# Performance work log

Measured on AMD Instinct MI355X. Metric: run time of the kernel, lower is better.

Reference implementation:

```python
import jax, jax.numpy as jnp
import numpy as np

D_MODEL = 2048
N_HEADS = 16
D_KEY = D_MODEL // N_HEADS
ALIBI_SLOPE = 8.0
KEY_SCALE = D_KEY ** -0.5
B, S = 2, 2048


def setup_inputs() -> dict:
    key = jax.random.key(0)
    ks = jax.random.split(key, 12)
    sd = D_MODEL ** -0.5
    return {
        "states": jax.random.normal(ks[0], (B, S, D_MODEL), jnp.float32),
        "bias_mask": jax.random.normal(ks[1], (B, S, S), jnp.float32),
        # weights stored [in, out] (torch Linear applies x @ W.T + b)
        "wq": jax.random.normal(ks[2], (D_MODEL, D_MODEL), jnp.float32) * sd,
        "bq": jnp.zeros((D_MODEL,), jnp.float32),
        "wk": jax.random.normal(ks[3], (D_MODEL, D_MODEL), jnp.float32) * sd,
        "bk": jnp.zeros((D_MODEL,), jnp.float32),
        "wv": jax.random.normal(ks[4], (D_MODEL, D_MODEL), jnp.float32) * sd,
        "bv": jnp.zeros((D_MODEL,), jnp.float32),
        "wg": jax.random.normal(ks[5], (D_MODEL, N_HEADS), jnp.float32) * sd,
        "bg": jnp.zeros((N_HEADS,), jnp.float32),
        "wo": jax.random.normal(ks[6], (D_MODEL, D_MODEL), jnp.float32) * sd,
        "bo": jnp.zeros((D_MODEL,), jnp.float32),
    }


def reference(states, bias_mask, wq, bq, wk, bk, wv, bv, wg, bg, wo, bo):
    # head_scale = exp2(-(h+1)*alibi_slope/n_heads), non-trainable buffer
    head_scale = jnp.exp2(-(jnp.arange(N_HEADS, dtype=jnp.float32) + 1.0)
                          * ALIBI_SLOPE / N_HEADS)
    # [B, H, Q, K] bias with per-head ALiBi scaling
    bias = bias_mask[:, None, :, :] * head_scale[None, :, None, None]

    def heads(x, w, b):  # [B,S,D] -> [B,H,S,Dk]
        y = x @ w + b
        return y.reshape(x.shape[0], x.shape[1], N_HEADS, D_KEY).transpose(0, 2, 1, 3)

    q = heads(states, wq, bq)
    k = heads(states, wk, bk)
    v = heads(states, wv, bv)

    scores = jnp.einsum('bhqd,bhkd->bhqk', q, k) * KEY_SCALE + bias
    probs = jax.nn.softmax(scores, axis=-1)
    o = jnp.einsum('bhqk,bhkd->bqhd', probs, v)  # [B,S,H,Dk]

    g = jax.nn.sigmoid(states @ wg + bg)  # [B,S,H] head gate
    o = o * g[..., None]

    return o.reshape(o.shape[0], o.shape[1], D_MODEL) @ wo + bo
```

## Files before the change

### kernel.cpp

```cpp
#include <hip/hip_runtime.h>
#include <hip/hip_bf16.h>

#define SEQ 2048
#define DM 2048
#define NH 16
#define DK 128
#define LOG2E 1.4426950408889634f
#define QK_SCALE 0.08838834764831845f

typedef __attribute__((ext_vector_type(8))) short short8;
typedef __attribute__((ext_vector_type(4))) float f32x4;
typedef __attribute__((ext_vector_type(4))) unsigned short us4;

__device__ __forceinline__ unsigned short f2b(float f) {
  union { float f; unsigned u; } v; v.f = f;
  unsigned r = v.u + 0x7fffu + ((v.u >> 16) & 1u);
  return (unsigned short)(r >> 16);
}
__device__ __forceinline__ float b2f(unsigned short v) {
  union { unsigned u; float f; } x; x.u = ((unsigned)v) << 16; return x.f;
}

__device__ __forceinline__ void gl_lds16(const void* g, void* l) {
  __builtin_amdgcn_global_load_lds((const __attribute__((address_space(1))) void*)g,
                                   (__attribute__((address_space(3))) void*)l, 16, 0, 0);
}

#define SBAR()   __builtin_amdgcn_s_barrier()
#define SCHED0() __builtin_amdgcn_sched_barrier(0)
#define LGKM0()  asm volatile("s_waitcnt lgkmcnt(0)" ::: "memory")

__global__ __launch_bounds__(256) void cast_bf16_kernel(const float* __restrict__ in,
                                                        unsigned short* __restrict__ out) {
  int i = blockIdx.x * 256 + threadIdx.x;
  const float4* p = (const float4*)in;
  float4 a = p[2*i], b = p[2*i+1];
  us4 r0, r1;
  r0[0]=f2b(a.x); r0[1]=f2b(a.y); r0[2]=f2b(a.z); r0[3]=f2b(a.w);
  r1[0]=f2b(b.x); r1[1]=f2b(b.y); r1[2]=f2b(b.z); r1[3]=f2b(b.w);
  us4* o = (us4*)out;
  o[2*i] = r0; o[2*i+1] = r1;
}

__global__ __launch_bounds__(256) void transpose_cast4_kernel(const float* __restrict__ w0,
                                                              const float* __restrict__ w1,
                                                              const float* __restrict__ w2,
                                                              const float* __restrict__ w3,
                                                              unsigned short* __restrict__ dst) {
  const float* w = (blockIdx.z == 0) ? w0 : (blockIdx.z == 1) ? w1 : (blockIdx.z == 2) ? w2 : w3;
  unsigned short* wt = dst + (size_t)blockIdx.z * DM * DM;
  __shared__ float t[64][65];
  int c0 = blockIdx.x * 64, r0 = blockIdx.y * 64;
  int tid = threadIdx.x;
  int rr = tid >> 4;
  int c4 = (tid & 15) * 4;
#pragma unroll
  for (int p = 0; p < 4; ++p) {
    int r = p*16 + rr;
    float4 v = *(const float4*)&w[(size_t)(r0 + r)*DM + c0 + c4];
    t[r][c4] = v.x; t[r][c4+1] = v.y; t[r][c4+2] = v.z; t[r][c4+3] = v.w;
  }
  __syncthreads();
#pragma unroll
  for (int p = 0; p < 4; ++p) {
    int c = p*16 + rr;
    us4 v;
    v[0] = f2b(t[c4+0][c]); v[1] = f2b(t[c4+1][c]);
    v[2] = f2b(t[c4+2][c]); v[3] = f2b(t[c4+3][c]);
    *(us4*)&wt[(size_t)(c0 + c)*DM + r0 + c4] = v;
  }
}

__global__ __launch_bounds__(256) void transpose_wg_kernel(const float* __restrict__ wg,
                                                           unsigned short* __restrict__ wgT) {
  int idx = blockIdx.x * 256 + threadIdx.x;
  int c = idx & 15;
  int r0 = (idx >> 4) * 4;
#pragma unroll
  for (int r = 0; r < 4; ++r)
    wgT[(size_t)c*DM + r0 + r] = f2b(wg[(size_t)(r0 + r)*NH + c]);
}

__device__ __forceinline__ void gemm256_core(const unsigned short* __restrict__ A,
                                             const unsigned short* __restrict__ Bt,
                                             int m0, int n0, f32x4 (&acc)[8][4]) {
  __shared__ __align__(16) unsigned short Ab[2][2][8192];
  __shared__ __align__(16) unsigned short Bb[2][2][8192];
  const int TK = DM / 64;

  int tid = threadIdx.x, wid = tid >> 6, lane = tid & 63;
  int lo = lane & 15, hi = lane >> 4;
  int wm = wid >> 2, wn = wid & 3;
  int w2 = wid * 2;

  int srow8 = lane >> 3;
  int skb = (((lane & 7) ^ srow8) << 4);
  const char* Ag = (const char*)A;
  const char* Bg = (const char*)Bt;

#define STG_A(S,CUR) do {                                                          \
    const char* g = Ag + (size_t)(S)*128 + skb;                                    \
    char* l = (char*)&Ab[CUR][0][0] + w2*1024;                                     \
    gl_lds16(g + (size_t)(m0 + w2*8 + srow8)*4096,           l);                   \
    gl_lds16(g + (size_t)(m0 + w2*8 + 8 + srow8)*4096,       l + 1024);            \
    gl_lds16(g + (size_t)(m0 + 128 + w2*8 + srow8)*4096,     l + 16384);           \
    gl_lds16(g + (size_t)(m0 + 128 + w2*8 + 8 + srow8)*4096, l + 16384 + 1024);    \
  } while(0)
#define STG_B(S,CUR) do {                                                          \
    const char* g = Bg + (size_t)(S)*128 + skb;                                    \
    char* l = (char*)&Bb[CUR][0][0] + w2*1024;                                     \
    gl_lds16(g + (size_t)(n0 + w2*8 + srow8)*4096,           l);                   \
    gl_lds16(g + (size_t)(n0 + w2*8 + 8 + srow8)*4096,       l + 1024);            \
    gl_lds16(g + (size_t)(n0 + 128 + w2*8 + srow8)*4096,     l + 16384);           \
    gl_lds16(g + (size_t)(n0 + 128 + w2*8 + 8 + srow8)*4096, l + 16384 + 1024);    \
  } while(0)

#pragma unroll
  for (int i = 0; i < 8; ++i)
#pragma unroll
    for (int j = 0; j < 4; ++j) acc[i][j] = (f32x4){0.f,0.f,0.f,0.f};

  STG_B(0,0); STG_A(0,0); STG_B(1,1); STG_A(1,1);
  asm volatile("s_waitcnt vmcnt(8)" ::: "memory");
  SBAR();

  int msk = (lo & 7) << 4;
  int k0 = (hi*16) ^ msk;
  int k1 = (64 + hi*16) ^ msk;
  int brow = (wn & 1) * 64;

  short8 a[4][2], bA[2][2], bB[2][2];

#define MF16(MH,NH,BF)                                                              \
  __builtin_amdgcn_s_setprio(1);                                                    \
  _Pragma("unroll") for (int mm = 0; mm < 4; ++mm)                                  \
  _Pragma("unroll") for (int nn = 0; nn < 2; ++nn) {                                \
    acc[(MH)*4+mm][(NH)*2+nn] = __builtin_amdgcn_mfma_f32_16x16x32_bf16(            \
        a[mm][0], BF[nn][0], acc[(MH)*4+mm][(NH)*2+nn], 0, 0, 0);                   \
    acc[(MH)*4+mm][(NH)*2+nn] = __builtin_amdgcn_mfma_f32_16x16x32_bf16(            \
        a[mm][1], BF[nn][1], acc[(MH)*4+mm][(NH)*2+nn], 0, 0, 0);                   \
  }                                                                                 \
  __builtin_amdgcn_s_setprio(0);

  for (int s = 0; s < TK; ++s) {
    int cur = s & 1;
    const char* Ac = (const char*)&Ab[cur][wm][0];
    const char* Bc = (const char*)&Bb[cur][wn >> 1][0];
    bool pre = (s + 2) < TK;

#pragma unroll
    for (int mm = 0; mm < 4; ++mm) {
      a[mm][0] = *(const short8*)(Ac + (mm*16 + lo)*128 + k0);
      a[mm][1] = *(const short8*)(Ac + (mm*16 + lo)*128 + k1);
    }
#pragma unroll
    for (int nn = 0; nn < 2; ++nn) {
      bA[nn][0] = *(const short8*)(Bc + (brow + nn*16 + lo)*128 + k0);
      bA[nn][1] = *(const short8*)(Bc + (brow + nn*16 + lo)*128 + k1);
    }
    SBAR(); LGKM0(); SCHED0();
    MF16(0, 0, bA);
    SBAR();

#pragma unroll
    for (int nn = 0; nn < 2; ++nn) {
      bB[nn][0] = *(const short8*)(Bc + (brow + (2+nn)*16 + lo)*128 + k0);
      bB[nn][1] = *(const short8*)(Bc + (brow + (2+nn)*16 + lo)*128 + k1);
    }
    SBAR(); LGKM0(); SCHED0();
    MF16(0, 1, bB);
    SBAR();

#pragma unroll
    for (int mm = 0; mm < 4; ++mm) {
      a[mm][0] = *(const short8*)(Ac + ((64 + mm*16 + lo)*128) + k0);
      a[mm][1] = *(const short8*)(Ac + ((64 + mm*16 + lo)*128) + k1);
    }
    if (pre) STG_B(s + 2, cur);
    SBAR(); LGKM0(); SCHED0();
    MF16(1, 0, bA);
    SBAR();

    if (pre) {
      STG_A(s + 2, cur);
      asm volatile("s_waitcnt vmcnt(8)" ::: "memory");
    } else if (s == TK - 2) {
      asm volatile("s_waitcnt vmcnt(0)" ::: "memory");
    }
    SBAR();
    MF16(1, 1, bB);
    SBAR();
  }
#undef STG_A
#undef STG_B
#undef MF16
}

__global__ __launch_bounds__(512, 2) void gemm256_qkv_kernel(const unsigned short* __restrict__ A,
                                                             const unsigned short* __restrict__ Bt,
                                                             const float* __restrict__ bq,
                                                             const float* __restrict__ bk,
                                                             const float* __restrict__ bv,
                                                             unsigned short* __restrict__ QB,
                                                             unsigned short* __restrict__ KB,
                                                             unsigned short* __restrict__ VTB) {
  f32x4 acc[8][4];
  int bid = blockIdx.x;
  int orig = (bid & 7) * 48 + (bid >> 3);
  int n0 = (orig % 24) * 256, m0 = (orig / 24) * 256;
  gemm256_core(A, Bt, m0, n0, acc);

  int tid = threadIdx.x, wid = tid >> 6, lane = tid & 63;
  int lo = lane & 15, hi = lane >> 4;
  int wm = wid >> 2, wn = wid & 3;
  int sect = n0 >> 11;

  if (sect == 2) {
#pragma unroll
    for (int mi = 0; mi < 8; ++mi) {
      int m = m0 + wm*128 + mi*16 + 4*hi;
      int b = m >> 11, srow = m & 2047;
#pragma unroll
      for (int nf = 0; nf < 4; ++nf) {
        int n = n0 + wn*64 + nf*16 + lo;
        int nl = n & 2047, h = nl >> 7, d = nl & 127;
        float bvv = bv[nl];
        us4 pk;
#pragma unroll
        for (int r = 0; r < 4; ++r) pk[r] = f2b(acc[mi][nf][r] + bvv);
        *(us4*)&VTB[(((size_t)(b*NH + h))*DK + d)*SEQ + srow] = pk;
      }
    }
  } else {
    unsigned short* out = sect ? KB : QB;
    const float* bp = sect ? bk : bq;
    const float qs = sect ? 1.f : QK_SCALE * LOG2E;
#pragma unroll
    for (int mi = 0; mi < 8; ++mi) {
#pragma unroll
      for (int nf = 0; nf < 4; ++nf) {
        int n = n0 + wn*64 + nf*16 + lo;
        int nl = n & 2047, h = nl >> 7, d = nl & 127;
        float bvv = bp[nl];
#pragma unroll
        for (int r = 0; r < 4; ++r) {
          int m = m0 + wm*128 + mi*16 + 4*hi + r;
          int b = m >> 11, srow = m & 2047;
          out[(((size_t)(b*NH + h))*SEQ + srow)*DK + d] = f2b((acc[mi][nf][r] + bvv) * qs);
        }
      }
    }
  }
}

__global__ __launch_bounds__(512, 2) void gemm256_ao_kernel(const unsigned short* __restrict__ A,
                                                            const unsigned short* __restrict__ Bt,
                                                            const float* __restrict__ bias,
                                                            float* __restrict__ out) {
  f32x4 acc[8][4];
  int bid = blockIdx.x;
  int orig = (bid & 7) * 16 + (bid >> 3);
  int n0 = (orig & 7) * 256, m0 = (orig >> 3) * 256;
  gemm256_core(A, Bt, m0, n0, acc);

  int tid = threadIdx.x, wid = tid >> 6, lane = tid & 63;
  int lo = lane & 15, hi = lane >> 4;
  int wm = wid >> 2, wn = wid & 3;
#pragma unroll
  for (int mi = 0; mi < 8; ++mi) {
#pragma unroll
    for (int nf = 0; nf < 4; ++nf) {
      int n = n0 + wn*64 + nf*16 + lo;
      float bvv = bias[n];
#pragma unroll
      for (int r = 0; r < 4; ++r) {
        int m = m0 + wm*128 + mi*16 + 4*hi + r;
        out[(size_t)m*DM + n] = acc[mi][nf][r] + bvv;
      }
    }
  }
}

__global__ __launch_bounds__(256) void gate_mfma_kernel(const unsigned short* __restrict__ XB,
                                                        const unsigned short* __restrict__ wgT,
                                                        const float* __restrict__ bg,
                                                        float* __restrict__ G) {
  int tid = threadIdx.x, wid = tid >> 6, lane = tid & 63;
  int lo = lane & 15, hi = lane >> 4;
  int m0 = blockIdx.x * 64 + wid * 16;

  f32x4 acc = {0.f, 0.f, 0.f, 0.f};
  const unsigned short* xrow = XB + (size_t)(m0 + lo) * DM + hi * 8;
  const unsigned short* grow = wgT + (size_t)lo * DM + hi * 8;
#pragma unroll 4
  for (int kt = 0; kt < DM; kt += 32) {
    short8 a = *(const short8*)(xrow + kt);
    short8 b = *(const short8*)(grow + kt);
    acc = __builtin_amdgcn_mfma_f32_16x16x32_bf16(a, b, acc, 0, 0, 0);
  }
  float bgv = bg[lo];
#pragma unroll
  for (int r = 0; r < 4; ++r) {
    float x = acc[r] + bgv;
    G[(size_t)(m0 + 4*hi + r) * NH + lo] = 1.f / (1.f + __builtin_amdgcn_exp2f(-x * LOG2E));
  }
}

__global__ __attribute__((amdgpu_flat_work_group_size(512,512)))
__attribute__((amdgpu_waves_per_eu(2,4)))
void attn_kernel(const unsigned short* __restrict__ Q,
                 const unsigned short* __restrict__ Kb,
                 const unsigned short* __restrict__ VT,
                 const unsigned short* __restrict__ biasb,
                 const float* __restrict__ G,
                 unsigned short* __restrict__ OG) {
  __shared__ __align__(16) unsigned short kbuf[2][64*128];
  __shared__ __align__(16) unsigned short vbuf[2][128*64];
  __shared__ __align__(16) unsigned short pbuf[8*16*64];

  int bid = blockIdx.x;
  int h  = bid & 15;
  int b  = (bid >> 4) & 1;
  int qt = bid >> 5;
  int bh = b*NH + h;

  int tid = threadIdx.x, wid = tid >> 6, lane = tid & 63;
  int lo = lane & 15, hi = lane >> 4;
  int qw0 = qt*128 + wid*16;

  float hs2 = __builtin_amdgcn_exp2f(-(float)(h+1) * 0.5f) * LOG2E;

  short8 qf[4];
#pragma unroll
  for (int ks = 0; ks < 4; ++ks)
    qf[ks] = *(const short8*)&Q[((size_t)bh*SEQ + qw0 + lo)*DK + ks*32 + hi*8];

  f32x4 zero4 = {0.f,0.f,0.f,0.f};
  f32x4 acco[8];
#pragma unroll
  for (int f = 0; f < 8; ++f) acco[f] = zero4;
  float lrun[4];
#pragma unroll
  for (int r = 0; r < 4; ++r) lrun[r] = 0.f;

  const char* kbase = (const char*)Kb + ((size_t)bh*SEQ)*DK*2;
  const char* vbase = (const char*)VT + ((size_t)bh*DK)*SEQ*2;
  const unsigned short* bb = biasb + ((size_t)b*SEQ + qw0 + 4*hi)*SEQ + lo;
  char* pb = (char*)pbuf + wid*2048;

  int s16 = lane >> 4, srow8 = lane >> 3;
  int kof = (lane & 15) * 16, vof = (lane & 7) * 16;
  int w2 = wid * 2;

#define STAGE_KV(KT, BUF) do {                                                        \
    _Pragma("unroll")                                                                 \
    for (int c = 0; c < 2; ++c) {                                                     \
      int krc = (w2 + c)*4 + s16;                                                     \
      gl_lds16(kbase + (size_t)((KT) + krc)*256 + (kof ^ ((krc & 7) << 4)),           \
               (char*)kbuf[BUF] + (w2 + c)*1024);                                     \
      int vrc = (w2 + c)*8 + srow8;                                                   \
      gl_lds16(vbase + (size_t)vrc*4096 + (size_t)(KT)*2 + (vof ^ (srow8 << 4)),      \
               (char*)vbuf[BUF] + (w2 + c)*1024);                                     \
    }                                                                                 \
  } while(0)

  unsigned short br[4][4];
#pragma unroll
  for (int r = 0; r < 4; ++r)
#pragma unroll
    for (int nf = 0; nf < 4; ++nf)
      br[r][nf] = bb[(size_t)r*SEQ + nf*16];
  STAGE_KV(0, 0);
  STAGE_KV(64, 1);
  asm volatile("s_waitcnt vmcnt(4)" ::: "memory");
  SBAR();

  const int NT = SEQ / 64;
  int cur = 0;
  for (int t = 0; t < NT; ++t) {
    f32x4 sf[4];
    __builtin_amdgcn_s_setprio(1);
#pragma unroll
    for (int nf = 0; nf < 4; ++nf) {
      f32x4 a = zero4;
#pragma unroll
      for (int ks = 0; ks < 4; ++ks) {
        int krw = nf*16 + lo;
        int cb = (ks*32 + hi*8)*2;
        short8 kf = *(const short8*)((const char*)kbuf[cur] + krw*256 + (cb ^ ((krw & 7) << 4)));
        a = __builtin_amdgcn_mfma_f32_16x16x32_bf16(qf[ks], kf, a, 0, 0, 0);
      }
      sf[nf] = a;
    }
    __builtin_amdgcn_s_setprio(0);

#pragma unroll
    for (int r = 0; r < 4; ++r) {
      int prow = 4*hi + r;
#pragma unroll
      for (int nf = 0; nf < 4; ++nf) {
        float s = fmaf(b2f(br[r][nf]), hs2, sf[nf][r]);
        float p = __builtin_amdgcn_exp2f(s);
        lrun[r] += p;
        *(unsigned short*)(pb + prow*128 + ((((nf*16 + lo)*2)) ^ ((prow & 7) << 4))) = f2b(p);
      }
    }

    short8 pf[2];
#pragma unroll
    for (int ks = 0; ks < 2; ++ks)
      pf[ks] = *(const short8*)(pb + lo*128 + ((ks*64 + hi*16) ^ ((lo & 7) << 4)));
    __builtin_amdgcn_s_setprio(1);
#pragma unroll
    for (int f = 0; f < 8; ++f) {
#pragma unroll
      for (int ks = 0; ks < 2; ++ks) {
        int vrw = f*16 + lo;
        int cb = (ks*32 + hi*8)*2;
        short8 vf = *(const short8*)((const char*)vbuf[cur] + vrw*128 + (cb ^ ((vrw & 7) << 4)));
        acco[f] = __builtin_amdgcn_mfma_f32_16x16x32_bf16(pf[ks], vf, acco[f], 0, 0, 0);
      }
    }
    __builtin_amdgcn_s_setprio(0);

    LGKM0(); SBAR();

    bool more1 = (t + 1) < NT;
    bool more2 = (t + 2) < NT;
    if (more1) {
      int ktn = (t + 1) * 64;
#pragma unroll
      for (int r = 0; r < 4; ++r)
#pragma unroll
        for (int nf = 0; nf < 4; ++nf)
          br[r][nf] = bb[(size_t)r*SEQ + ktn + nf*16];
    }
    if (more2) {
      STAGE_KV((t + 2) * 64, cur);
      asm volatile("s_waitcnt vmcnt(20)" ::: "memory");
    } else if (more1) {
      asm volatile("s_waitcnt vmcnt(16)" ::: "memory");
    }
    SBAR();
    cur ^= 1;
  }
#undef STAGE_KV

#pragma unroll
  for (int r = 0; r < 4; ++r) {
    float l = lrun[r];
    l += __shfl_xor(l, 1); l += __shfl_xor(l, 2);
    l += __shfl_xor(l, 4); l += __shfl_xor(l, 8);
    lrun[r] = l;
  }

#pragma unroll
  for (int r = 0; r < 4; ++r) {
    int qrow = qw0 + 4*hi + r;
    float inv = 1.f / lrun[r];
    float g = G[((size_t)(b*SEQ + qrow))*NH + h];
    float sgl = inv * g;
#pragma unroll
    for (int f = 0; f < 8; ++f)
      OG[((size_t)(b*SEQ) + qrow)*DM + h*DK + f*16 + lo] = f2b(acco[f][r] * sgl);
  }
}

extern "C" void kernel_launch(void* const* d_in, const int* in_sizes, int n_in,
                              void* d_out, int out_size, void* d_ws, size_t ws_size,
                              hipStream_t stream) {
  const float* states    = (const float*)d_in[0];
  const float* bias_mask = (const float*)d_in[1];
  const float* wq = (const float*)d_in[2];
  const float* bq = (const float*)d_in[3];
  const float* wk = (const float*)d_in[4];
  const float* bk = (const float*)d_in[5];
  const float* wv = (const float*)d_in[6];
  const float* bv = (const float*)d_in[7];
  const float* wg = (const float*)d_in[8];
  const float* bg = (const float*)d_in[9];
  const float* wo = (const float*)d_in[10];
  const float* bo = (const float*)d_in[11];

  char* ws = (char*)d_ws;
  unsigned short* XB   = (unsigned short*)(ws + 0);
  unsigned short* OGB  = XB;
  unsigned short* WQVT = (unsigned short*)(ws + 16777216UL);
  unsigned short* WOT  = (unsigned short*)(ws + 41943040UL);
  unsigned short* QB   = (unsigned short*)(ws + 50331648UL);
  unsigned short* KB   = (unsigned short*)(ws + 67108864UL);
  unsigned short* VTB  = (unsigned short*)(ws + 83886080UL);
  unsigned short* BIASB= (unsigned short*)(ws + 100663296UL);
  float*          GB   = (float*)         (ws + 117440512UL);
  unsigned short* WGT  = (unsigned short*)(ws + 117702656UL);

  cast_bf16_kernel<<<4096, 256, 0, stream>>>(states, XB);
  cast_bf16_kernel<<<4096, 256, 0, stream>>>(bias_mask, BIASB);
  transpose_cast4_kernel<<<dim3(32, 32, 4), 256, 0, stream>>>(wq, wk, wv, wo, WQVT);
  transpose_wg_kernel<<<32, 256, 0, stream>>>(wg, WGT);

  gemm256_qkv_kernel<<<384, 512, 0, stream>>>(XB, WQVT, bq, bk, bv, QB, KB, VTB);

  gate_mfma_kernel<<<64, 256, 0, stream>>>(XB, WGT, bg, GB);

  attn_kernel<<<512, 512, 0, stream>>>(QB, KB, VTB, BIASB, GB, OGB);

  gemm256_ao_kernel<<<128, 512, 0, stream>>>(OGB, WOT, bo, (float*)d_out);
}
```

Measured before the change: 378.7 us.

## Shrink GEMM tiles to 128x256 and merge the two cast launches

The shared bf16 GEMM core goes from 256x256 to 128x256 output tiles, so each wave now covers 64 rows instead of 128. The A-tile LDS staging is halved and the vmcnt wait counts are adjusted to match. The QKV and output-projection GEMMs now launch on 2D grids with more blocks, so more CUs have work, especially the output projection, which previously had only 128 blocks. The custom block-order swizzle is dropped. The two fp32-to-bf16 cast launches are merged into one kernel, at the cost of lower reuse of B tiles per block and possibly worse L2 locality.

```diff
diff --git a/kernel.cpp b/kernel.cpp
--- a/kernel.cpp
+++ b/kernel.cpp
@@ -30,9 +30,14 @@
 #define SCHED0() __builtin_amdgcn_sched_barrier(0)
 #define LGKM0()  asm volatile("s_waitcnt lgkmcnt(0)" ::: "memory")
 
-__global__ __launch_bounds__(256) void cast_bf16_kernel(const float* __restrict__ in,
-                                                        unsigned short* __restrict__ out) {
-  int i = blockIdx.x * 256 + threadIdx.x;
+__global__ __launch_bounds__(256) void cast2_bf16_kernel(const float* __restrict__ in0,
+                                                         unsigned short* __restrict__ out0,
+                                                         const float* __restrict__ in1,
+                                                         unsigned short* __restrict__ out1) {
+  int bid = blockIdx.x;
+  const float* in = (bid < 4096) ? in0 : in1;
+  unsigned short* out = (bid < 4096) ? out0 : out1;
+  int i = ((bid < 4096) ? bid : bid - 4096) * 256 + threadIdx.x;
   const float4* p = (const float4*)in;
   float4 a = p[2*i], b = p[2*i+1];
   us4 r0, r1;
@@ -81,10 +86,10 @@
     wgT[(size_t)c*DM + r0 + r] = f2b(wg[(size_t)(r0 + r)*NH + c]);
 }
 
-__device__ __forceinline__ void gemm256_core(const unsigned short* __restrict__ A,
+__device__ __forceinline__ void gemm128_core(const unsigned short* __restrict__ A,
                                              const unsigned short* __restrict__ Bt,
-                                             int m0, int n0, f32x4 (&acc)[8][4]) {
-  __shared__ __align__(16) unsigned short Ab[2][2][8192];
+                                             int m0, int n0, f32x4 (&acc)[4][4]) {
+  __shared__ __align__(16) unsigned short Ab[2][8192];
   __shared__ __align__(16) unsigned short Bb[2][2][8192];
   const int TK = DM / 64;
 
@@ -100,11 +105,9 @@
 
 #define STG_A(S,CUR) do {                                                          \
     const char* g = Ag + (size_t)(S)*128 + skb;                                    \
-    char* l = (char*)&Ab[CUR][0][0] + w2*1024;                                     \
-    gl_lds16(g + (size_t)(m0 + w2*8 + srow8)*4096,           l);                   \
-    gl_lds16(g + (size_t)(m0 + w2*8 + 8 + srow8)*4096,       l + 1024);            \
-    gl_lds16(g + (size_t)(m0 + 128 + w2*8 + srow8)*4096,     l + 16384);           \
-    gl_lds16(g + (size_t)(m0 + 128 + w2*8 + 8 + srow8)*4096, l + 16384 + 1024);    \
+    char* l = (char*)&Ab[CUR][0] + w2*1024;                                        \
+    gl_lds16(g + (size_t)(m0 + w2*8 + srow8)*4096,     l);                         \
+    gl_lds16(g + (size_t)(m0 + w2*8 + 8 + srow8)*4096, l + 1024);                  \
   } while(0)
 #define STG_B(S,CUR) do {                                                          \
     const char* g = Bg + (size_t)(S)*128 + skb;                                    \
@@ -116,12 +119,12 @@
   } while(0)
 
 #pragma unroll
-  for (int i = 0; i < 8; ++i)
+  for (int i = 0; i < 4; ++i)
 #pragma unroll
     for (int j = 0; j < 4; ++j) acc[i][j] = (f32x4){0.f,0.f,0.f,0.f};
 
   STG_B(0,0); STG_A(0,0); STG_B(1,1); STG_A(1,1);
-  asm volatile("s_waitcnt vmcnt(8)" ::: "memory");
+  asm volatile("s_waitcnt vmcnt(6)" ::: "memory");
   SBAR();
 
   int msk = (lo & 7) << 4;
@@ -131,27 +134,27 @@
 
   short8 a[4][2], bA[2][2], bB[2][2];
 
-#define MF16(MH,NH,BF)                                                              \
+#define MF8(MH,NHH,BF)                                                              \
   __builtin_amdgcn_s_setprio(1);                                                    \
-  _Pragma("unroll") for (int mm = 0; mm < 4; ++mm)                                  \
+  _Pragma("unroll") for (int mm = 0; mm < 2; ++mm)                                  \
   _Pragma("unroll") for (int nn = 0; nn < 2; ++nn) {                                \
-    acc[(MH)*4+mm][(NH)*2+nn] = __builtin_amdgcn_mfma_f32_16x16x32_bf16(            \
-        a[mm][0], BF[nn][0], acc[(MH)*4+mm][(NH)*2+nn], 0, 0, 0);                   \
-    acc[(MH)*4+mm][(NH)*2+nn] = __builtin_amdgcn_mfma_f32_16x16x32_bf16(            \
-        a[mm][1], BF[nn][1], acc[(MH)*4+mm][(NH)*2+nn], 0, 0, 0);                   \
+    acc[(MH)*2+mm][(NHH)*2+nn] = __builtin_amdgcn_mfma_f32_16x16x32_bf16(           \
+        a[(MH)*2+mm][0], BF[nn][0], acc[(MH)*2+mm][(NHH)*2+nn], 0, 0, 0);           \
+    acc[(MH)*2+mm][(NHH)*2+nn] = __builtin_amdgcn_mfma_f32_16x16x32_bf16(           \
+        a[(MH)*2+mm][1], BF[nn][1], acc[(MH)*2+mm][(NHH)*2+nn], 0, 0, 0);           \
   }                                                                                 \
   __builtin_amdgcn_s_setprio(0);
 
   for (int s = 0; s < TK; ++s) {
     int cur = s & 1;
-    const char* Ac = (const char*)&Ab[cur][wm][0];
+    const char* Ac = (const char*)&Ab[cur][0];
     const char* Bc = (const char*)&Bb[cur][wn >> 1][0];
     bool pre = (s + 2) < TK;
 
 #pragma unroll
     for (int mm = 0; mm < 4; ++mm) {
-      a[mm][0] = *(const short8*)(Ac + (mm*16 + lo)*128 + k0);
-      a[mm][1] = *(const short8*)(Ac + (mm*16 + lo)*128 + k1);
+      a[mm][0] = *(const short8*)(Ac + (wm*64 + mm*16 + lo)*128 + k0);
+      a[mm][1] = *(const short8*)(Ac + (wm*64 + mm*16 + lo)*128 + k1);
     }
 #pragma unroll
     for (int nn = 0; nn < 2; ++nn) {
@@ -159,7 +162,7 @@
       bA[nn][1] = *(const short8*)(Bc + (brow + nn*16 + lo)*128 + k1);
     }
     SBAR(); LGKM0(); SCHED0();
-    MF16(0, 0, bA);
+    MF8(0, 0, bA);
     SBAR();
 
 #pragma unroll
@@ -168,35 +171,30 @@
       bB[nn][1] = *(const short8*)(Bc + (brow + (2+nn)*16 + lo)*128 + k1);
     }
     SBAR(); LGKM0(); SCHED0();
-    MF16(0, 1, bB);
-    SBAR();
-
-#pragma unroll
-    for (int mm = 0; mm < 4; ++mm) {
-      a[mm][0] = *(const short8*)(Ac + ((64 + mm*16 + lo)*128) + k0);
-      a[mm][1] = *(const short8*)(Ac + ((64 + mm*16 + lo)*128) + k1);
-    }
+    MF8(0, 1, bB);
+    SBAR();
+
     if (pre) STG_B(s + 2, cur);
-    SBAR(); LGKM0(); SCHED0();
-    MF16(1, 0, bA);
+    SBAR();
+    MF8(1, 0, bA);
     SBAR();
 
     if (pre) {
       STG_A(s + 2, cur);
-      asm volatile("s_waitcnt vmcnt(8)" ::: "memory");
+      asm volatile("s_waitcnt vmcnt(6)" ::: "memory");
     } else if (s == TK - 2) {
       asm volatile("s_waitcnt vmcnt(0)" ::: "memory");
     }
     SBAR();
-    MF16(1, 1, bB);
+    MF8(1, 1, bB);
     SBAR();
   }
 #undef STG_A
 #undef STG_B
-#undef MF16
-}
-
-__global__ __launch_bounds__(512, 2) void gemm256_qkv_kernel(const unsigned short* __restrict__ A,
+#undef MF8
+}
+
+__global__ __launch_bounds__(512, 2) void gemm128_qkv_kernel(const unsigned short* __restrict__ A,
                                                              const unsigned short* __restrict__ Bt,
                                                              const float* __restrict__ bq,
                                                              const float* __restrict__ bk,
@@ -204,25 +202,25 @@
                                                              unsigned short* __restrict__ QB,
                                                              unsigned short* __restrict__ KB,
                                                              unsigned short* __restrict__ VTB) {
-  f32x4 acc[8][4];
-  int bid = blockIdx.x;
-  int orig = (bid & 7) * 48 + (bid >> 3);
-  int n0 = (orig % 24) * 256, m0 = (orig / 24) * 256;
-  gemm256_core(A, Bt, m0, n0, acc);
+  f32x4 acc[4][4];
+  int n0 = blockIdx.x * 256, m0 = blockIdx.y * 128;
+  gemm128_core(A, Bt, m0, n0, acc);
 
   int tid = threadIdx.x, wid = tid >> 6, lane = tid & 63;
   int lo = lane & 15, hi = lane >> 4;
   int wm = wid >> 2, wn = wid & 3;
+  int m_base = m0 + wm*64;
+  int n_base = n0 + wn*64;
   int sect = n0 >> 11;
 
   if (sect == 2) {
 #pragma unroll
-    for (int mi = 0; mi < 8; ++mi) {
-      int m = m0 + wm*128 + mi*16 + 4*hi;
+    for (int mi = 0; mi < 4; ++mi) {
+      int m = m_base + mi*16 + 4*hi;
       int b = m >> 11, srow = m & 2047;
 #pragma unroll
       for (int nf = 0; nf < 4; ++nf) {
-        int n = n0 + wn*64 + nf*16 + lo;
+        int n = n_base + nf*16 + lo;
         int nl = n & 2047, h = nl >> 7, d = nl & 127;
         float bvv = bv[nl];
         us4 pk;
@@ -236,15 +234,15 @@
     const float* bp = sect ? bk : bq;
     const float qs = sect ? 1.f : QK_SCALE * LOG2E;
 #pragma unroll
-    for (int mi = 0; mi < 8; ++mi) {
+    for (int mi = 0; mi < 4; ++mi) {
 #pragma unroll
       for (int nf = 0; nf < 4; ++nf) {
-        int n = n0 + wn*64 + nf*16 + lo;
+        int n = n_base + nf*16 + lo;
         int nl = n & 2047, h = nl >> 7, d = nl & 127;
         float bvv = bp[nl];
 #pragma unroll
         for (int r = 0; r < 4; ++r) {
-          int m = m0 + wm*128 + mi*16 + 4*hi + r;
+          int m = m_base + mi*16 + 4*hi + r;
           int b = m >> 11, srow = m & 2047;
           out[(((size_t)(b*NH + h))*SEQ + srow)*DK + d] = f2b((acc[mi][nf][r] + bvv) * qs);
         }
@@ -253,28 +251,26 @@
   }
 }
 
-__global__ __launch_bounds__(512, 2) void gemm256_ao_kernel(const unsigned short* __restrict__ A,
+__global__ __launch_bounds__(512, 2) void gemm128_ao_kernel(const unsigned short* __restrict__ A,
                                                             const unsigned short* __restrict__ Bt,
                                                             const float* __restrict__ bias,
                                                             float* __restrict__ out) {
-  f32x4 acc[8][4];
-  int bid = blockIdx.x;
-  int orig = (bid & 7) * 16 + (bid >> 3);
-  int n0 = (orig & 7) * 256, m0 = (orig >> 3) * 256;
-  gemm256_core(A, Bt, m0, n0, acc);
+  f32x4 acc[4][4];
+  int n0 = blockIdx.x * 256, m0 = blockIdx.y * 128;
+  gemm128_core(A, Bt, m0, n0, acc);
 
   int tid = threadIdx.x, wid = tid >> 6, lane = tid & 63;
   int lo = lane & 15, hi = lane >> 4;
   int wm = wid >> 2, wn = wid & 3;
 #pragma unroll
-  for (int mi = 0; mi < 8; ++mi) {
+  for (int mi = 0; mi < 4; ++mi) {
 #pragma unroll
     for (int nf = 0; nf < 4; ++nf) {
       int n = n0 + wn*64 + nf*16 + lo;
       float bvv = bias[n];
 #pragma unroll
       for (int r = 0; r < 4; ++r) {
-        int m = m0 + wm*128 + mi*16 + 4*hi + r;
+        int m = m0 + wm*64 + mi*16 + 4*hi + r;
         out[(size_t)m*DM + n] = acc[mi][nf][r] + bvv;
       }
     }
@@ -494,16 +490,15 @@
   float*          GB   = (float*)         (ws + 117440512UL);
   unsigned short* WGT  = (unsigned short*)(ws + 117702656UL);
 
-  cast_bf16_kernel<<<4096, 256, 0, stream>>>(states, XB);
-  cast_bf16_kernel<<<4096, 256, 0, stream>>>(bias_mask, BIASB);
+  cast2_bf16_kernel<<<8192, 256, 0, stream>>>(states, XB, bias_mask, BIASB);
   transpose_cast4_kernel<<<dim3(32, 32, 4), 256, 0, stream>>>(wq, wk, wv, wo, WQVT);
   transpose_wg_kernel<<<32, 256, 0, stream>>>(wg, WGT);
 
-  gemm256_qkv_kernel<<<384, 512, 0, stream>>>(XB, WQVT, bq, bk, bv, QB, KB, VTB);
+  gemm128_qkv_kernel<<<dim3(24, 32), 512, 0, stream>>>(XB, WQVT, bq, bk, bv, QB, KB, VTB);
 
   gate_mfma_kernel<<<64, 256, 0, stream>>>(XB, WGT, bg, GB);
 
   attn_kernel<<<512, 512, 0, stream>>>(QB, KB, VTB, BIASB, GB, OGB);
 
-  gemm256_ao_kernel<<<128, 512, 0, stream>>>(OGB, WOT, bo, (float*)d_out);
-}
+  gemm128_ao_kernel<<<dim3(8, 32), 512, 0, stream>>>(OGB, WOT, bo, (float*)d_out);
+}
```

Result: faster. 356.5 us (-5.8%).
